# Performance work log

Measured on AMD Instinct MI355X. Metric: run time of the kernel, lower is better.

The kernel has to match this reference:

```python
import jax, jax.numpy as jnp
import numpy as np

B, T = 4096, 16384
KLEN = 50          # min(50, n_steps) with dt=1
REFRACTORY = 3.0   # self.refractory / self.dt


def setup_inputs() -> dict:
    key = jax.random.key(0)
    k1, = jax.random.split(key, 1)
    # scale so that v_reset + I_filtered/100 can cross v_th (=-55 vs reset -70)
    I_input = jax.random.normal(k1, (B, T), dtype=jnp.float32) * 2000.0
    return {
        "I_input": I_input,
        "tau_m": jnp.float32(10.0),
        "tau_s": jnp.float32(5.0),
        "v_th": jnp.float32(-55.0),
        "v_reset": jnp.float32(-70.0),
        "eta": jnp.float32(-5.0),
    }


def _srm_spikes(I_input, tau_m, tau_s, v_th, v_reset, eta):
    # synaptic kernel: (exp(-t/tau_m) - exp(-t/tau_s)) / sum
    t = jnp.arange(KLEN, dtype=jnp.float32)
    kernel = jnp.exp(-t / tau_m) - jnp.exp(-t / tau_s)
    kernel = kernel / (jnp.sum(kernel) + 1e-10)
    # 'same' convolution per trace (np.convolve semantics: kernel flipped)
    I_filt = jax.vmap(lambda x: jnp.convolve(x, kernel, mode="same"))(I_input)

    def step(ref, I_t):
        # ref: [B] refractory countdown; I_t: [B] filtered current at time t
        in_ref = ref > 0
        v_free = v_reset + I_t / 100.0
        spike = jnp.where(jnp.logical_and(~in_ref, v_free >= v_th), 1.0, 0.0)
        new_ref = jnp.where(in_ref, ref - 1.0,
                            jnp.where(spike > 0, REFRACTORY, 0.0))
        return new_ref, spike

    ref0 = jnp.zeros((I_input.shape[0],), dtype=jnp.float32)
    # original loop runs t = 1 .. n_steps-1; spikes[0] stays 0
    _, spikes_t = jax.lax.scan(step, ref0, jnp.swapaxes(I_filt[:, 1:], 0, 1))
    spikes = jnp.concatenate(
        [jnp.zeros((I_input.shape[0], 1), dtype=jnp.float32),
         jnp.swapaxes(spikes_t, 0, 1)], axis=1)
    return spikes


def reference(I_input, tau_m, tau_s, v_th, v_reset, eta):
    return _srm_spikes(I_input, tau_m, tau_s, v_th, v_reset, eta)
```

## Files before the change

kernel.cpp:

```cpp
#include <hip/hip_runtime.h>


#define TLEN   16384
#define NROWS  4096
#define KLEN   50
#define WPB    4
#define SEGS   16
#define SEGLEN 1024

#define FGRP  256
#define FNGRP 64
#define TILEW 336

#define WS_FLAGS_OFF 256
#define WS_NEED (WS_FLAGS_OFF + (size_t)NROWS * SEGS * sizeof(int))

typedef float f4 __attribute__((ext_vector_type(4)));

__device__ __forceinline__ float uniformf(float x) {
    return __int_as_float(__builtin_amdgcn_readfirstlane(__float_as_int(x)));
}

__device__ __forceinline__ int map_compose(int first, int then) {
    int r = 0;
#pragma unroll
    for (int s = 0; s < 4; ++s) {
        int a = (first >> (2 * s)) & 3;
        int b = (then >> (2 * a)) & 3;
        r |= b << (2 * s);
    }
    return r;
}

__device__ float solve_thresh(float v_reset, float v_th) {
    auto tokey = [](float f) {
        unsigned u = __float_as_uint(f);
        return (u & 0x80000000u) ? ~u : (u | 0x80000000u);
    };
    auto fromkey = [](unsigned k) {
        unsigned u = (k & 0x80000000u) ? (k & 0x7FFFFFFFu) : ~k;
        return __uint_as_float(u);
    };
    const float maxf = 3.402823466e38f;
    unsigned lo = tokey(-maxf), hi = tokey(maxf);
    if (!((v_reset + maxf / 100.0f) >= v_th))
        return __uint_as_float(0x7F800000u);
    while (lo < hi) {
        unsigned mid = lo + ((hi - lo) >> 1);
        float a = fromkey(mid);
        if ((v_reset + a / 100.0f) >= v_th) hi = mid;
        else lo = mid + 1;
    }
    return fromkey(lo);
}

__global__ __launch_bounds__(64)
void setup_kernel(const float* __restrict__ p_tau_m,
                  const float* __restrict__ p_tau_s,
                  const float* __restrict__ p_v_th,
                  const float* __restrict__ p_v_reset,
                  double* __restrict__ wsd)
{
    if (threadIdx.x != 0) return;
    const double tm = (double)p_tau_m[0];
    const double ts = (double)p_tau_s[0];
    const double Ad  = exp(-1.0 / tm);
    const double Bd  = exp(-1.0 / ts);
    const double A50 = exp(-50.0 / tm);
    const double B50 = exp(-50.0 / ts);
    const double S = (1.0 - A50) / (1.0 - Ad) - (1.0 - B50) / (1.0 - Bd);
    const float athr = solve_thresh(p_v_reset[0], p_v_th[0]);
    wsd[0] = Ad;
    wsd[1] = Bd;
    wsd[2] = A50;
    wsd[3] = B50;
    wsd[4] = (double)athr * (S + 1e-10);
}

__global__ __launch_bounds__(256)
void conv_kernel(const float* __restrict__ I,
                 const double* __restrict__ wsd,
                 float* __restrict__ out,
                 int* __restrict__ flags)
{
    const int lane = threadIdx.x & 63;
    const int wid  = threadIdx.x >> 6;
    const int wg   = blockIdx.x * WPB + wid;
    const int row  = wg >> 4;
    const int seg  = wg & 15;

    const double Ad    = wsd[0];
    const double Bd    = wsd[1];
    const double A50   = wsd[2];
    const double B50   = wsd[3];
    const double athrS = wsd[4];

    const float* Irow = I + (size_t)row * TLEN;
    float* Orow = out + (size_t)row * TLEN;

    const int pos0 = seg * SEGLEN;
    const int t0   = pos0 + 16 * lane;
    const int off  = t0 - 28;

    f4 wv[17];
    if (off >= 0 && off <= TLEN - 68) {
#pragma unroll
        for (int i = 0; i < 17; ++i)
            wv[i] = *(const f4*)(Irow + off + 4 * i);
    } else {
#pragma unroll
        for (int i = 0; i < 17; ++i) {
            const int idx = off + 4 * i;
            wv[i] = (idx >= 0 && idx <= TLEN - 4)
                        ? *(const f4*)(Irow + idx)
                        : (f4){0.0f, 0.0f, 0.0f, 0.0f};
        }
    }
#define WIN(m) ((double)wv[(m) >> 2][(m) & 3])

    double pa = 0.0, pb = 0.0;
#pragma unroll
    for (int j = 49; j >= 0; --j) {
        const double xx = WIN(52 - j);
        pa = fma(Ad, pa, xx);
        pb = fma(Bd, pb, xx);
    }

    int m16 = ((pa - pb) >= athrS) ? 1 : 0;

#pragma unroll
    for (int k = 1; k < 16; ++k) {
        const double xk = WIN(52 + k);
        const double lk = WIN(2 + k);
        pa = fma(Ad, pa, fma(-A50, lk, xk));
        pb = fma(Bd, pb, fma(-B50, lk, xk));
        m16 |= ((pa - pb) >= athrS) ? (1 << k) : 0;
    }
#undef WIN

    if (t0 == 0) m16 &= ~1;
    const int rowflag = m16;

    const int sh = 4 * (lane & 3);
#pragma unroll
    for (int j = 0; j < 4; ++j) {
        const int bits = __shfl(m16, (lane >> 2) + 16 * j, 64);
        f4 o0;
        o0.x = ((bits >> (sh + 0)) & 1) ? 1.0f : 0.0f;
        o0.y = ((bits >> (sh + 1)) & 1) ? 1.0f : 0.0f;
        o0.z = ((bits >> (sh + 2)) & 1) ? 1.0f : 0.0f;
        o0.w = ((bits >> (sh + 3)) & 1) ? 1.0f : 0.0f;
        __builtin_nontemporal_store(o0, (f4*)(Orow + pos0 + 4 * lane + 256 * j));
    }

    const unsigned long long anyb = __ballot(rowflag != 0);
    if (lane == 0) flags[wg] = (anyb != 0ULL) ? 1 : 0;
}

__global__ __launch_bounds__(256)
void fixup_kernel(const int* __restrict__ flags,
                  float* __restrict__ out)
{
    const int lane = threadIdx.x & 63;
    const int wid  = threadIdx.x >> 6;
    const int row  = blockIdx.x * WPB + wid;

    const int* pf = flags + SEGS * row;
    int any = 0;
#pragma unroll
    for (int j = 0; j < SEGS; ++j) any |= pf[j];
    if (any == 0) return;

    float* Orow = out + (size_t)row * TLEN;
    int r0 = 0;

    for (int g = 0; g < FNGRP; ++g) {
        f4 o = *(const f4*)(Orow + g * FGRP + 4 * lane);
        int cand[4];
        cand[0] = (o.x != 0.0f);
        cand[1] = (o.y != 0.0f);
        cand[2] = (o.z != 0.0f);
        cand[3] = (o.w != 0.0f);

        const int cm = cand[0] | cand[1] | cand[2] | cand[3];
        const unsigned long long anyc = __ballot(cm != 0);
        if (anyc == 0ULL) { r0 = 0; continue; }

        int s0 = 0, s1 = 1, s2 = 2, s3 = 3;
#pragma unroll
        for (int k = 0; k < 4; ++k) {
            const int c3 = cand[k] ? 3 : 0;
            s0 = (s0 > 0) ? (s0 - 1) : c3;
            s1 = (s1 > 0) ? (s1 - 1) : c3;
            s2 = (s2 > 0) ? (s2 - 1) : c3;
            s3 = (s3 > 0) ? (s3 - 1) : c3;
        }
        int P = s0 | (s1 << 2) | (s2 << 4) | (s3 << 6);

#pragma unroll
        for (int d = 1; d < 64; d <<= 1) {
            const int prev = __shfl_up(P, d, 64);
            const int comp = map_compose(prev, P);
            P = (lane >= d) ? comp : P;
        }
        const int Pprev = __shfl_up(P, 1, 64);
        const int sin0  = (lane == 0) ? r0 : ((Pprev >> (2 * r0)) & 3);
        const int Pfull = __shfl(P, 63, 64);
        r0 = (Pfull >> (2 * r0)) & 3;

        int s = sin0;
        float sp[4];
#pragma unroll
        for (int k = 0; k < 4; ++k) {
            const int spike = (s == 0) & cand[k];
            sp[k] = spike ? 1.0f : 0.0f;
            s = (s > 0) ? (s - 1) : (cand[k] ? 3 : 0);
        }
        f4 o0; o0.x = sp[0]; o0.y = sp[1]; o0.z = sp[2]; o0.w = sp[3];
        *(f4*)(Orow + g * FGRP + 4 * lane) = o0;
    }
}

__global__ __launch_bounds__(256)
void srm_kernel(const float* __restrict__ I,
                const float* __restrict__ p_tau_m,
                const float* __restrict__ p_tau_s,
                const float* __restrict__ p_v_th,
                const float* __restrict__ p_v_reset,
                float* __restrict__ out)
{
    __shared__ __align__(16) float tile[WPB][2][TILEW];

    const int lane = threadIdx.x & 63;
    const int wid  = threadIdx.x >> 6;
    const int row  = blockIdx.x * WPB + wid;

    const float tau_m   = p_tau_m[0];
    const float tau_s   = p_tau_s[0];
    const float v_th    = p_v_th[0];
    const float v_reset = p_v_reset[0];

    float ku[KLEN];
    float ksum = 0.0f;
#pragma unroll
    for (int t = 0; t < KLEN; ++t) {
        float ft = (float)t;
        float v = expf(-ft / tau_m) - expf(-ft / tau_s);
        ksum += v;
        ku[t] = uniformf(v);
    }
    const float kden = uniformf(ksum + 1e-10f);
    float kt[KLEN];
#pragma unroll
    for (int t = 0; t < KLEN; ++t) kt[t] = uniformf(ku[t] / kden);

    const float athr = uniformf(solve_thresh(v_reset, v_th));

    const float* Irow = I + (size_t)row * TLEN;
    float* Orow = out + (size_t)row * TLEN;

    float Cv[4], Nv[4], Lv[4];
    {
        f4 a = *(const f4*)(Irow + 0 * FGRP + 4 * lane);
        Cv[0] = a.x; Cv[1] = a.y; Cv[2] = a.z; Cv[3] = a.w;
        f4 c = *(const f4*)(Irow + 1 * FGRP + 4 * lane);
        Nv[0] = c.x; Nv[1] = c.y; Nv[2] = c.z; Nv[3] = c.w;
    }

    if (lane < 8) {
        f4 z = (f4){0.0f, 0.0f, 0.0f, 0.0f};
        *(f4*)&tile[wid][0][4 * lane] = z;
    }
    {
        f4 c; c.x = Cv[0]; c.y = Cv[1]; c.z = Cv[2]; c.w = Cv[3];
        *(f4*)&tile[wid][0][32 + 4 * lane] = c;
    }

    int r0 = 0;

    for (int g = 0; g < FNGRP; ++g) {
        const int cur = g & 1;
        const int nxt = cur ^ 1;

        if (g + 2 < FNGRP) {
            f4 a = *(const f4*)(Irow + (size_t)(g + 2) * FGRP + 4 * lane);
            Lv[0] = a.x; Lv[1] = a.y; Lv[2] = a.z; Lv[3] = a.w;
        } else {
            Lv[0] = Lv[1] = Lv[2] = Lv[3] = 0.0f;
        }

        f4 nv; nv.x = Nv[0]; nv.y = Nv[1]; nv.z = Nv[2]; nv.w = Nv[3];
        if (lane < 8)
            *(f4*)&tile[wid][cur][288 + 4 * lane] = nv;
        *(f4*)&tile[wid][nxt][32 + 4 * lane] = nv;
        if (lane >= 56) {
            f4 cv; cv.x = Cv[0]; cv.y = Cv[1]; cv.z = Cv[2]; cv.w = Cv[3];
            *(f4*)&tile[wid][nxt][4 * (lane - 56)] = cv;
        }

        f4 wv[15];
#pragma unroll
        for (int i = 0; i < 15; ++i)
            wv[i] = *(const f4*)&tile[wid][cur][4 * lane + 4 + 4 * i];
#define WIN(m) (wv[(m) >> 2][(m) & 3])

        float acc[4];
        acc[0] = acc[1] = acc[2] = acc[3] = 0.0f;
#pragma unroll
        for (int o = -25; o <= 27; ++o) {
            const float w = WIN(o + 28);
#pragma unroll
            for (int k = 0; k < 4; ++k) {
                const int jj = k + 24 - o;
                if (jj >= 0 && jj < KLEN)
                    acc[k] = fmaf(kt[jj], w, acc[k]);
            }
        }
#undef WIN

        const int tb = g * FGRP + 4 * lane;
        int cand[4];
#pragma unroll
        for (int k = 0; k < 4; ++k)
            cand[k] = (acc[k] >= athr) ? 1 : 0;
        cand[0] &= (tb != 0);

        const int cm = cand[0] | cand[1] | cand[2] | cand[3];
        const unsigned long long anyc = __ballot(cm != 0);

        f4 o0;
        if (anyc == 0ULL) {
            o0 = (f4){0.0f, 0.0f, 0.0f, 0.0f};
            r0 = 0;
        } else {
            int s0 = 0, s1 = 1, s2 = 2, s3 = 3;
#pragma unroll
            for (int k = 0; k < 4; ++k) {
                const int c3 = cand[k] ? 3 : 0;
                s0 = (s0 > 0) ? (s0 - 1) : c3;
                s1 = (s1 > 0) ? (s1 - 1) : c3;
                s2 = (s2 > 0) ? (s2 - 1) : c3;
                s3 = (s3 > 0) ? (s3 - 1) : c3;
            }
            int P = s0 | (s1 << 2) | (s2 << 4) | (s3 << 6);
#pragma unroll
            for (int d = 1; d < 64; d <<= 1) {
                const int prev = __shfl_up(P, d, 64);
                const int comp = map_compose(prev, P);
                P = (lane >= d) ? comp : P;
            }
            const int Pprev = __shfl_up(P, 1, 64);
            const int sin0  = (lane == 0) ? r0 : ((Pprev >> (2 * r0)) & 3);
            const int Pfull = __shfl(P, 63, 64);
            r0 = (Pfull >> (2 * r0)) & 3;

            int s = sin0;
            float sp[4];
#pragma unroll
            for (int k = 0; k < 4; ++k) {
                const int spike = (s == 0) & cand[k];
                sp[k] = spike ? 1.0f : 0.0f;
                s = (s > 0) ? (s - 1) : (cand[k] ? 3 : 0);
            }
            o0.x = sp[0]; o0.y = sp[1]; o0.z = sp[2]; o0.w = sp[3];
        }

        __builtin_nontemporal_store(o0, (f4*)(Orow + tb));

#pragma unroll
        for (int j = 0; j < 4; ++j) { Cv[j] = Nv[j]; Nv[j] = Lv[j]; }
    }
}

extern "C" void kernel_launch(void* const* d_in, const int* in_sizes, int n_in,
                              void* d_out, int out_size, void* d_ws, size_t ws_size,
                              hipStream_t stream) {
    const float* I       = (const float*)d_in[0];
    const float* tau_m   = (const float*)d_in[1];
    const float* tau_s   = (const float*)d_in[2];
    const float* v_th    = (const float*)d_in[3];
    const float* v_reset = (const float*)d_in[4];
    float* out = (float*)d_out;

    if (ws_size >= WS_NEED) {
        double* wsd = (double*)d_ws;
        int* flags  = (int*)((char*)d_ws + WS_FLAGS_OFF);
        setup_kernel<<<dim3(1), dim3(64), 0, stream>>>(
            tau_m, tau_s, v_th, v_reset, wsd);
        conv_kernel<<<dim3(NROWS * SEGS / WPB), dim3(256), 0, stream>>>(
            I, wsd, out, flags);
        fixup_kernel<<<dim3(NROWS / WPB), dim3(256), 0, stream>>>(flags, out);
    } else {
        srm_kernel<<<dim3(NROWS / WPB), dim3(256), 0, stream>>>(
            I, tau_m, tau_s, v_th, v_reset, out);
    }
}
```

Before: 147.6 us.

## Replace FP64 recursive filter with direct FP32 convolution; drop nontemporal stores

The conv kernel used a double-precision two-exponential recursive filter to compute the filtered current. It now computes the 50-tap kernel explicitly in float in setup and evaluates the convolution directly in FP32 with 16 accumulators per lane. This removes the serial FP64 FMA chain, which is slow relative to FP32, at the cost of about 800 FP32 FMAs per lane and possible rounding differences near the threshold. Output stores also switch from nontemporal to regular stores.

```diff
diff --git a/kernel.cpp b/kernel.cpp
--- a/kernel.cpp
+++ b/kernel.cpp
@@ -59,27 +59,28 @@
                   const float* __restrict__ p_tau_s,
                   const float* __restrict__ p_v_th,
                   const float* __restrict__ p_v_reset,
-                  double* __restrict__ wsd)
+                  float* __restrict__ wsf)
 {
-    if (threadIdx.x != 0) return;
-    const double tm = (double)p_tau_m[0];
-    const double ts = (double)p_tau_s[0];
-    const double Ad  = exp(-1.0 / tm);
-    const double Bd  = exp(-1.0 / ts);
-    const double A50 = exp(-50.0 / tm);
-    const double B50 = exp(-50.0 / ts);
-    const double S = (1.0 - A50) / (1.0 - Ad) - (1.0 - B50) / (1.0 - Bd);
-    const float athr = solve_thresh(p_v_reset[0], p_v_th[0]);
-    wsd[0] = Ad;
-    wsd[1] = Bd;
-    wsd[2] = A50;
-    wsd[3] = B50;
-    wsd[4] = (double)athr * (S + 1e-10);
+    const int lane = threadIdx.x & 63;
+    const float tau_m = p_tau_m[0];
+    const float tau_s = p_tau_s[0];
+
+    float ft = (float)lane;
+    float v = (lane < KLEN) ? (expf(-ft / tau_m) - expf(-ft / tau_s)) : 0.0f;
+
+    float ksum = 0.0f;
+    for (int t = 0; t < KLEN; ++t)
+        ksum += __shfl(v, t, 64);
+    const float kden = ksum + 1e-10f;
+    const float kt = v / kden;
+
+    if (lane < KLEN) wsf[lane] = kt;
+    if (lane == 0)   wsf[KLEN] = solve_thresh(p_v_reset[0], p_v_th[0]);
 }
 
 __global__ __launch_bounds__(256)
 void conv_kernel(const float* __restrict__ I,
-                 const double* __restrict__ wsd,
+                 const float* __restrict__ wsf,
                  float* __restrict__ out,
                  int* __restrict__ flags)
 {
@@ -89,11 +90,10 @@
     const int row  = wg >> 4;
     const int seg  = wg & 15;
 
-    const double Ad    = wsd[0];
-    const double Bd    = wsd[1];
-    const double A50   = wsd[2];
-    const double B50   = wsd[3];
-    const double athrS = wsd[4];
+    float kt[KLEN];
+#pragma unroll
+    for (int t = 0; t < KLEN; ++t) kt[t] = wsf[t];
+    const float athr = wsf[KLEN];
 
     const float* Irow = I + (size_t)row * TLEN;
     float* Orow = out + (size_t)row * TLEN;
@@ -116,28 +116,27 @@
                         : (f4){0.0f, 0.0f, 0.0f, 0.0f};
         }
     }
-#define WIN(m) ((double)wv[(m) >> 2][(m) & 3])
-
-    double pa = 0.0, pb = 0.0;
-#pragma unroll
-    for (int j = 49; j >= 0; --j) {
-        const double xx = WIN(52 - j);
-        pa = fma(Ad, pa, xx);
-        pb = fma(Bd, pb, xx);
-    }
-
-    int m16 = ((pa - pb) >= athrS) ? 1 : 0;
-
-#pragma unroll
-    for (int k = 1; k < 16; ++k) {
-        const double xk = WIN(52 + k);
-        const double lk = WIN(2 + k);
-        pa = fma(Ad, pa, fma(-A50, lk, xk));
-        pb = fma(Bd, pb, fma(-B50, lk, xk));
-        m16 |= ((pa - pb) >= athrS) ? (1 << k) : 0;
+#define WIN(m) (wv[(m) >> 2][(m) & 3])
+
+    float acc[16];
+#pragma unroll
+    for (int k = 0; k < 16; ++k) acc[k] = 0.0f;
+#pragma unroll
+    for (int o = -25; o <= 39; ++o) {
+        const float wx = WIN(o + 28);
+#pragma unroll
+        for (int k = 0; k < 16; ++k) {
+            const int jj = k + 24 - o;
+            if (jj >= 0 && jj < KLEN)
+                acc[k] = fmaf(kt[jj], wx, acc[k]);
+        }
     }
 #undef WIN
 
+    int m16 = 0;
+#pragma unroll
+    for (int k = 0; k < 16; ++k)
+        m16 |= (acc[k] >= athr) ? (1 << k) : 0;
     if (t0 == 0) m16 &= ~1;
     const int rowflag = m16;
 
@@ -150,7 +149,7 @@
         o0.y = ((bits >> (sh + 1)) & 1) ? 1.0f : 0.0f;
         o0.z = ((bits >> (sh + 2)) & 1) ? 1.0f : 0.0f;
         o0.w = ((bits >> (sh + 3)) & 1) ? 1.0f : 0.0f;
-        __builtin_nontemporal_store(o0, (f4*)(Orow + pos0 + 4 * lane + 256 * j));
+        *(f4*)(Orow + pos0 + 4 * lane + 256 * j) = o0;
     }
 
     const unsigned long long anyb = __ballot(rowflag != 0);
@@ -365,7 +364,7 @@
             o0.x = sp[0]; o0.y = sp[1]; o0.z = sp[2]; o0.w = sp[3];
         }
 
-        __builtin_nontemporal_store(o0, (f4*)(Orow + tb));
+        *(f4*)(Orow + tb) = o0;
 
 #pragma unroll
         for (int j = 0; j < 4; ++j) { Cv[j] = Nv[j]; Nv[j] = Lv[j]; }
@@ -383,12 +382,12 @@
     float* out = (float*)d_out;
 
     if (ws_size >= WS_NEED) {
-        double* wsd = (double*)d_ws;
+        float* wsf  = (float*)d_ws;
         int* flags  = (int*)((char*)d_ws + WS_FLAGS_OFF);
         setup_kernel<<<dim3(1), dim3(64), 0, stream>>>(
-            tau_m, tau_s, v_th, v_reset, wsd);
+            tau_m, tau_s, v_th, v_reset, wsf);
         conv_kernel<<<dim3(NROWS * SEGS / WPB), dim3(256), 0, stream>>>(
-            I, wsd, out, flags);
+            I, wsf, out, flags);
         fixup_kernel<<<dim3(NROWS / WPB), dim3(256), 0, stream>>>(flags, out);
     } else {
         srm_kernel<<<dim3(NROWS / WPB), dim3(256), 0, stream>>>(
```

Result: slower. 160.1 us (+8.5%).
